# Kernel tuning notes

Measured on AMD Instinct MI355X. Metric: run time of the kernel, lower is better.

## Reference

```python
import jax, jax.numpy as jnp
import numpy as np

B, S, D, H = 2, 2048, 2048, 16
DK = D // H


def setup_inputs() -> dict:
    key = jax.random.key(0)
    k1, k2, k3 = jax.random.split(key, 3)
    x = jax.random.normal(k1, (B, S, D), dtype=jnp.float32)
    # trunc-normal in the original; plain normal with matching std is fine for a numeric baseline
    std_qkv = 2.0 / (DK + D)  # note: original passes variance as std to trunc_normal_
    W_qkv = jax.random.normal(k2, (3 * D, D), dtype=jnp.float32) * std_qkv
    W_o = jax.random.normal(k3, (D, D), dtype=jnp.float32) * (1.0 / D)
    return {"x": x, "W_qkv": W_qkv, "W_o": W_o}


def reference(x, W_qkv, W_o):
    b, s, d = x.shape
    # fused QKV projection: y = x @ W_qkv^T
    qkv = jnp.einsum('bsd,ed->bse', x, W_qkv)  # [b, s, 3d]
    q, k, v = jnp.split(qkv, 3, axis=-1)
    # [b, s, d] -> [b, h, s, dk]
    def to_heads(t):
        return t.reshape(b, s, H, DK).transpose(0, 2, 1, 3)
    q, k, v = to_heads(q), to_heads(k), to_heads(v)
    scores = jnp.einsum('bhqd,bhkd->bhqk', q, k) / np.sqrt(DK).astype(np.float32)
    causal = jnp.tril(jnp.ones((s, s), dtype=bool))
    scores = jnp.where(causal, scores, -jnp.inf)
    att = jax.nn.softmax(scores, axis=-1)
    out = jnp.einsum('bhqk,bhkd->bhqd', att, v)  # [b, h, s, dk]
    out = out.transpose(0, 2, 1, 3).reshape(b, s, d)
    return jnp.einsum('bsd,od->bso', out, W_o)
```

## Files before the change

kernel.cpp:

```cpp
#include <hip/hip_runtime.h>

typedef _Float16 f16;
typedef _Float16 f16x4 __attribute__((ext_vector_type(4)));
typedef _Float16 f16x8 __attribute__((ext_vector_type(8)));
typedef float    f32x4 __attribute__((ext_vector_type(4)));

#define MFMA_F16(a,b,c) __builtin_amdgcn_mfma_f32_16x16x32_f16((a),(b),(c),0,0,0)

static constexpr int B_  = 2;
static constexpr int S_  = 2048;
static constexpr int D_  = 2048;
static constexpr int H_  = 16;
static constexpr int DK_ = 128;
static constexpr int K_  = 2048;

__device__ __forceinline__ void gload_lds16(const void* g, void* l) {
  __builtin_amdgcn_global_load_lds(
      (const __attribute__((address_space(1))) void*)g,
      (__attribute__((address_space(3))) void*)l, 16, 0, 0);
}

__global__ __launch_bounds__(256) void cast_f16_kernel(const float* __restrict__ in,
                                                       f16* __restrict__ out, int n4) {
  int i = blockIdx.x * 256 + threadIdx.x;
  int stride = gridDim.x * 256;
  for (int j = i; j < n4; j += stride) {
    float4 v = reinterpret_cast<const float4*>(in)[j];
    f16x4 o = {(f16)v.x, (f16)v.y, (f16)v.z, (f16)v.w};
    reinterpret_cast<f16x4*>(out)[j] = o;
  }
}


__device__ __forceinline__ void stage_ph(const f16* gA, const f16* gB, int t,
                                         char* slot, int w) {
  gload_lds16(gA + (size_t)(w * 16) * K_ + t * 32,       slot + w * 1024);
  gload_lds16(gB + (size_t)(w * 16) * K_ + t * 32,       slot + 8192 + w * 1024);
  gload_lds16(gB + (size_t)((w + 8) * 16) * K_ + t * 32, slot + 8192 + (w + 8) * 1024);
}

__device__ __forceinline__ void mfma_ph(const char* slot, int aoff, int boff, int lro,
                                        f32x4 (&acc)[4][4]) {
  f16x8 af[4], bf[4];
#pragma unroll
  for (int mi = 0; mi < 4; ++mi)
    af[mi] = *(const f16x8*)(slot + aoff + mi * 1024 + lro);
#pragma unroll
  for (int ni = 0; ni < 4; ++ni)
    bf[ni] = *(const f16x8*)(slot + boff + ni * 1024 + lro);
  __builtin_amdgcn_s_setprio(1);
#pragma unroll
  for (int mi = 0; mi < 4; ++mi)
#pragma unroll
    for (int ni = 0; ni < 4; ++ni)
      acc[mi][ni] = MFMA_F16(af[mi], bf[ni], acc[mi][ni]);
  __builtin_amdgcn_s_setprio(0);
}

#define SYNCW(N)                                              \
  asm volatile("s_waitcnt vmcnt(" #N ")" ::: "memory");       \
  __builtin_amdgcn_s_barrier();                               \
  asm volatile("" ::: "memory");

__device__ __forceinline__ void gemm_core_w8(const f16* __restrict__ A,
                                             const f16* __restrict__ Bw,
                                             int brow, int bcol, char* lds,
                                             f32x4 (&acc)[4][4]) {
  const int tid = threadIdx.x;
  const int w = tid >> 6, l = tid & 63;
  const int lg = l >> 4, lr = l & 15;
  const int wm = w >> 2, wn = w & 3;
  const int lro = (lr * 4 + (lg ^ ((lr >> 1) & 3))) * 16;
  const int aoff = wm * 4096;
  const int boff = 8192 + wn * 4096;

#pragma unroll
  for (int mi = 0; mi < 4; ++mi)
#pragma unroll
    for (int ni = 0; ni < 4; ++ni) acc[mi][ni] = (f32x4){0.f, 0.f, 0.f, 0.f};

  const int kgsrc = (l & 3) ^ ((l >> 3) & 3);
  const f16* gA = A  + (size_t)(brow * 128 + (l >> 2)) * K_ + kgsrc * 8;
  const f16* gB = Bw + (size_t)(bcol * 256 + (l >> 2)) * K_ + kgsrc * 8;

  char* s0 = lds;
  char* s1 = lds + 24576;
  char* s2 = lds + 49152;
  char* s3 = lds + 73728;

  stage_ph(gA, gB, 0, s0, w);
  stage_ph(gA, gB, 1, s1, w);
  stage_ph(gA, gB, 2, s2, w);
  SYNCW(6)

  for (int tb = 0; tb < 15; ++tb) {
    const int t = tb * 4;
    stage_ph(gA, gB, t + 3, s3, w); mfma_ph(s0, aoff, boff, lro, acc); SYNCW(6)
    stage_ph(gA, gB, t + 4, s0, w); mfma_ph(s1, aoff, boff, lro, acc); SYNCW(6)
    stage_ph(gA, gB, t + 5, s1, w); mfma_ph(s2, aoff, boff, lro, acc); SYNCW(6)
    stage_ph(gA, gB, t + 6, s2, w); mfma_ph(s3, aoff, boff, lro, acc); SYNCW(6)
  }
  stage_ph(gA, gB, 63, s3, w); mfma_ph(s0, aoff, boff, lro, acc); SYNCW(6)
  mfma_ph(s1, aoff, boff, lro, acc); SYNCW(3)
  mfma_ph(s2, aoff, boff, lro, acc); SYNCW(0)
  mfma_ph(s3, aoff, boff, lro, acc);
}

__global__ __launch_bounds__(512) void gemm_qkv_kernel(const f16* __restrict__ xb,
                                                       const f16* __restrict__ wqkv,
                                                       f16* __restrict__ Q,
                                                       f16* __restrict__ Kk,
                                                       f16* __restrict__ Vt) {
  __shared__ __align__(16) char lds[98304];
  const int bid = blockIdx.x;
  const int xcd = bid & 7;
  const int local = bid >> 3;
  const int brow = xcd * 4 + (local & 3);
  const int bcol = local >> 2;

  f32x4 acc[4][4];
  gemm_core_w8(xb, wqkv, brow, bcol, lds, acc);

  const int tid = threadIdx.x;
  const int w = tid >> 6, l = tid & 63;
  const int lg = l >> 4, lr = l & 15;
  const int wm = w >> 2, wn = w & 3;

  const int which = bcol >> 3;
  const int nsec = (bcol & 7) * 256;

  if (which == 2) {
#pragma unroll
    for (int mi = 0; mi < 4; ++mi) {
      const int m0 = brow * 128 + wm * 64 + mi * 16 + lg * 4;
      const int b = m0 >> 11, s = m0 & 2047;
#pragma unroll
      for (int ni = 0; ni < 4; ++ni) {
        const int n = nsec + wn * 64 + ni * 16 + lr;
        const int h = n >> 7, dk = n & 127;
        f16x4 v = {(f16)acc[mi][ni][0], (f16)acc[mi][ni][1],
                   (f16)acc[mi][ni][2], (f16)acc[mi][ni][3]};
        *(f16x4*)(Vt + ((size_t)(b * H_ + h) * DK_ + dk) * S_ + s) = v;
      }
    }
  } else {
    f16* outp = (which == 0) ? Q : Kk;
    const float scale = (which == 0) ? 0.08838834764831845f : 1.0f;
#pragma unroll
    for (int mi = 0; mi < 4; ++mi) {
      const int m0 = brow * 128 + wm * 64 + mi * 16 + lg * 4;
#pragma unroll
      for (int ni = 0; ni < 4; ++ni) {
        const int n = nsec + wn * 64 + ni * 16 + lr;
        const int h = n >> 7, dk = n & 127;
#pragma unroll
        for (int r = 0; r < 4; ++r) {
          const int mm = m0 + r;
          const int b = mm >> 11, s = mm & 2047;
          outp[(((size_t)b * H_ + h) * S_ + s) * DK_ + dk] = (f16)(acc[mi][ni][r] * scale);
        }
      }
    }
  }
}

__global__ __launch_bounds__(512) void gemm_out_kernel(const f16* __restrict__ ab,
                                                       const f16* __restrict__ wo,
                                                       float* __restrict__ out) {
  __shared__ __align__(16) char lds[98304];
  const int bid = blockIdx.x;
  const int xcd = bid & 7;
  const int local = bid >> 3;
  const int brow = xcd * 4 + (local & 3);
  const int bcol = local >> 2;

  f32x4 acc[4][4];
  gemm_core_w8(ab, wo, brow, bcol, lds, acc);

  const int tid = threadIdx.x;
  const int w = tid >> 6, l = tid & 63;
  const int lg = l >> 4, lr = l & 15;
  const int wm = w >> 2, wn = w & 3;

#pragma unroll
  for (int mi = 0; mi < 4; ++mi) {
    const int m0 = brow * 128 + wm * 64 + mi * 16 + lg * 4;
#pragma unroll
    for (int ni = 0; ni < 4; ++ni) {
      const int n = bcol * 256 + wn * 64 + ni * 16 + lr;
#pragma unroll
      for (int r = 0; r < 4; ++r)
        out[(size_t)(m0 + r) * D_ + n] = acc[mi][ni][r];
    }
  }
}

__global__ __launch_bounds__(256) void attn_kernel(const f16* __restrict__ Q,
                                                   const f16* __restrict__ Kg,
                                                   const f16* __restrict__ Vt,
                                                   f16* __restrict__ O) {
  __shared__ __align__(16) unsigned char Ks[64 * 256];
  __shared__ __align__(16) unsigned char Vs[128 * 128];
  __shared__ __align__(16) unsigned char Ps[4][16 * 128];

  const int bid = blockIdx.x;
  const int pr = bid & 15;
  const int h  = (bid >> 4) & 15;
  const int b  = bid >> 8;
  const int bh = b * H_ + h;
  const int tid = threadIdx.x;
  const int w = tid >> 6, l = tid & 63;
  const int lg = l >> 4, lr = l & 15;

  for (int half = 0; half < 2; ++half) {
    const int qt = half ? (31 - pr) : pr;

    const f16* Qg = Q + ((size_t)bh * S_ + qt * 64 + w * 16) * DK_;
    f16x8 qf[4];
#pragma unroll
    for (int kd = 0; kd < 4; ++kd)
      qf[kd] = *(const f16x8*)(Qg + (size_t)lr * DK_ + kd * 32 + lg * 8);

    f32x4 o[8];
#pragma unroll
    for (int n = 0; n < 8; ++n) o[n] = (f32x4){0.f, 0.f, 0.f, 0.f};
    float mrun[4] = {-1e30f, -1e30f, -1e30f, -1e30f};
    float lrun[4] = {0.f, 0.f, 0.f, 0.f};

    const int ntiles = qt + 1;
    for (int kt = 0; kt < ntiles; ++kt) {
      __syncthreads();
      const f16* Kt = Kg + ((size_t)bh * S_ + kt * 64) * DK_;
#pragma unroll
      for (int i = 0; i < 4; ++i) {
        const int chunk = i * 256 + tid;
        const int row = chunk >> 4, c8 = chunk & 15;
        uint4 v = *(const uint4*)(Kt + (size_t)row * DK_ + c8 * 8);
        *(uint4*)(Ks + row * 256 + ((c8 * 16) ^ ((row & 7) << 4))) = v;
      }
      const f16* Vtt = Vt + (size_t)bh * DK_ * S_ + kt * 64;
#pragma unroll
      for (int i = 0; i < 4; ++i) {
        const int chunk = i * 256 + tid;
        const int row = chunk >> 3, c8 = chunk & 7;
        uint4 v = *(const uint4*)(Vtt + (size_t)row * S_ + c8 * 8);
        *(uint4*)(Vs + row * 128 + ((c8 * 16) ^ ((row & 7) << 4))) = v;
      }
      __syncthreads();

      f32x4 s[4];
#pragma unroll
      for (int j = 0; j < 4; ++j) s[j] = (f32x4){0.f, 0.f, 0.f, 0.f};
      __builtin_amdgcn_s_setprio(1);
#pragma unroll
      for (int j = 0; j < 4; ++j) {
        const int row = j * 16 + lr;
#pragma unroll
        for (int kd = 0; kd < 4; ++kd) {
          f16x8 kf = *(const f16x8*)(Ks + row * 256 + ((kd * 64 + lg * 16) ^ ((row & 7) << 4)));
          s[j] = MFMA_F16(qf[kd], kf, s[j]);
        }
      }
      __builtin_amdgcn_s_setprio(0);
      if (kt == qt) {
#pragma unroll
        for (int j = 0; j < 4; ++j) {
          const int col = j * 16 + lr;
#pragma unroll
          for (int r = 0; r < 4; ++r) {
            const int qrow = w * 16 + lg * 4 + r;
            if (col > qrow) s[j][r] = -1e30f;
          }
        }
      }
      float scl[4];
#pragma unroll
      for (int r = 0; r < 4; ++r) {
        float m0 = fmaxf(fmaxf(s[0][r], s[1][r]), fmaxf(s[2][r], s[3][r]));
#pragma unroll
        for (int msk = 1; msk < 16; msk <<= 1) m0 = fmaxf(m0, __shfl_xor(m0, msk, 64));
        const float nm = fmaxf(mrun[r], m0);
        scl[r] = __expf(mrun[r] - nm);
        mrun[r] = nm;
      }
      float rs[4] = {0.f, 0.f, 0.f, 0.f};
#pragma unroll
      for (int j = 0; j < 4; ++j) {
#pragma unroll
        for (int r = 0; r < 4; ++r) {
          const float p = __expf(fmaxf(s[j][r] - mrun[r], -80.f));
          rs[r] += p;
          const int row = lg * 4 + r;
          const int cb = (j * 16 + lr) * 2;
          *(f16*)(Ps[w] + row * 128 + (cb ^ ((row & 7) << 4))) = (f16)p;
        }
      }
#pragma unroll
      for (int r = 0; r < 4; ++r) {
        float t = rs[r];
#pragma unroll
        for (int msk = 1; msk < 16; msk <<= 1) t += __shfl_xor(t, msk, 64);
        lrun[r] = lrun[r] * scl[r] + t;
      }
#pragma unroll
      for (int n = 0; n < 8; ++n)
#pragma unroll
        for (int r = 0; r < 4; ++r) o[n][r] *= scl[r];

      asm volatile("s_waitcnt lgkmcnt(0)" ::: "memory");

      __builtin_amdgcn_s_setprio(1);
#pragma unroll
      for (int ks = 0; ks < 2; ++ks) {
        f16x8 pf = *(const f16x8*)(Ps[w] + lr * 128 + ((ks * 64 + lg * 16) ^ ((lr & 7) << 4)));
#pragma unroll
        for (int n = 0; n < 8; ++n) {
          const int row = n * 16 + lr;
          f16x8 vf = *(const f16x8*)(Vs + row * 128 + ((ks * 64 + lg * 16) ^ ((row & 7) << 4)));
          o[n] = MFMA_F16(pf, vf, o[n]);
        }
      }
      __builtin_amdgcn_s_setprio(0);
    }

#pragma unroll
    for (int r = 0; r < 4; ++r) {
      const float inv = 1.0f / lrun[r];
      const int srow = qt * 64 + w * 16 + lg * 4 + r;
      f16* op = O + ((size_t)b * S_ + srow) * D_ + h * DK_;
#pragma unroll
      for (int n = 0; n < 8; ++n) op[n * 16 + lr] = (f16)(o[n][r] * inv);
    }
  }
}

extern "C" void kernel_launch(void* const* d_in, const int* in_sizes, int n_in,
                              void* d_out, int out_size, void* d_ws, size_t ws_size,
                              hipStream_t stream) {
  const float* x    = (const float*)d_in[0];
  const float* wqkv = (const float*)d_in[1];
  const float* wo   = (const float*)d_in[2];
  float* out = (float*)d_out;
  char* ws = (char*)d_ws;

  f16* xb     = (f16*)(ws + 0);
  f16* wqkvb  = (f16*)(ws + 16777216);
  f16* wob    = (f16*)(ws + 41943040);
  f16* Qb     = (f16*)(ws + 50331648);
  f16* Kb     = (f16*)(ws + 67108864);
  f16* Vtb    = (f16*)(ws + 83886080);
  f16* attn_o = (f16*)(ws + 0);

  cast_f16_kernel<<<2048, 256, 0, stream>>>(x, xb, 8388608 / 4);
  cast_f16_kernel<<<2048, 256, 0, stream>>>(wqkv, wqkvb, 12582912 / 4);
  cast_f16_kernel<<<1024, 256, 0, stream>>>(wo, wob, 4194304 / 4);

  gemm_qkv_kernel<<<768, 512, 0, stream>>>(xb, wqkvb, Qb, Kb, Vtb);
  attn_kernel<<<512, 256, 0, stream>>>(Qb, Kb, Vtb, attn_o);
  gemm_out_kernel<<<256, 512, 0, stream>>>(attn_o, wob, out);
}
```

Before: 269.9 us.

## Shrink GEMM tiles to 128x128 with double buffering, prefetch attention K/V, merge casts

Both GEMMs move from 128x256 tiles with a 4-stage LDS pipeline to 128x128 tiles with a 64-wide K step and a two-slot double buffer. This halves LDS per block and doubles the grid, so more blocks can be resident per CU. The attention kernel now loads the next K/V tile into registers while computing on the current one, and the three cast launches become a single kernel. The trade-off is lower arithmetic intensity per tile, a full vmcnt(0) wait at every stage, and more register pressure in attention.

```diff
diff --git a/kernel.cpp b/kernel.cpp
--- a/kernel.cpp
+++ b/kernel.cpp
@@ -20,114 +20,127 @@
       (__attribute__((address_space(3))) void*)l, 16, 0, 0);
 }
 
-__global__ __launch_bounds__(256) void cast_f16_kernel(const float* __restrict__ in,
-                                                       f16* __restrict__ out, int n4) {
+__global__ __launch_bounds__(256) void cast_all_kernel(const float* __restrict__ x,
+                                                       const float* __restrict__ wqkv,
+                                                       const float* __restrict__ wo,
+                                                       f16* __restrict__ xb,
+                                                       f16* __restrict__ wqkvb,
+                                                       f16* __restrict__ wob) {
+  const int total = 6291456;
   int i = blockIdx.x * 256 + threadIdx.x;
   int stride = gridDim.x * 256;
-  for (int j = i; j < n4; j += stride) {
-    float4 v = reinterpret_cast<const float4*>(in)[j];
+  for (int j = i; j < total; j += stride) {
+    const float* src; f16* dst; int jj;
+    if (j < 2097152)      { src = x;    dst = xb;    jj = j; }
+    else if (j < 5242880) { src = wqkv; dst = wqkvb; jj = j - 2097152; }
+    else                  { src = wo;   dst = wob;   jj = j - 5242880; }
+    float4 v = reinterpret_cast<const float4*>(src)[jj];
     f16x4 o = {(f16)v.x, (f16)v.y, (f16)v.z, (f16)v.w};
-    reinterpret_cast<f16x4*>(out)[j] = o;
-  }
-}
-
-
-__device__ __forceinline__ void stage_ph(const f16* gA, const f16* gB, int t,
-                                         char* slot, int w) {
-  gload_lds16(gA + (size_t)(w * 16) * K_ + t * 32,       slot + w * 1024);
-  gload_lds16(gB + (size_t)(w * 16) * K_ + t * 32,       slot + 8192 + w * 1024);
-  gload_lds16(gB + (size_t)((w + 8) * 16) * K_ + t * 32, slot + 8192 + (w + 8) * 1024);
-}
-
-__device__ __forceinline__ void mfma_ph(const char* slot, int aoff, int boff, int lro,
-                                        f32x4 (&acc)[4][4]) {
-  f16x8 af[4], bf[4];
+    reinterpret_cast<f16x4*>(dst)[jj] = o;
+  }
+}
+
+
+#define SYNCW0                                          \
+  asm volatile("s_waitcnt vmcnt(0)" ::: "memory");      \
+  __builtin_amdgcn_s_barrier();                         \
+  asm volatile("" ::: "memory");
+
+__device__ __forceinline__ void stage2(const f16* gA, const f16* gB, char* slot, int w) {
+  gload_lds16(gA,      slot +         w * 1024);
+  gload_lds16(gA + 32, slot +  8192 + w * 1024);
+  gload_lds16(gB,      slot + 16384 + w * 1024);
+  gload_lds16(gB + 32, slot + 24576 + w * 1024);
+}
+
+__device__ __forceinline__ void compute2(const char* slot, int aoff, int boff, int lro,
+                                         f32x4 (&acc)[4][2]) {
+  f16x8 a0[4], b0[2], a1[4], b1[2];
+#pragma unroll
+  for (int mi = 0; mi < 4; ++mi) {
+    a0[mi] = *(const f16x8*)(slot +        aoff + mi * 1024 + lro);
+    a1[mi] = *(const f16x8*)(slot + 8192 + aoff + mi * 1024 + lro);
+  }
+#pragma unroll
+  for (int ni = 0; ni < 2; ++ni) {
+    b0[ni] = *(const f16x8*)(slot + 16384 + boff + ni * 1024 + lro);
+    b1[ni] = *(const f16x8*)(slot + 24576 + boff + ni * 1024 + lro);
+  }
+  __builtin_amdgcn_s_setprio(1);
 #pragma unroll
   for (int mi = 0; mi < 4; ++mi)
-    af[mi] = *(const f16x8*)(slot + aoff + mi * 1024 + lro);
-#pragma unroll
-  for (int ni = 0; ni < 4; ++ni)
-    bf[ni] = *(const f16x8*)(slot + boff + ni * 1024 + lro);
-  __builtin_amdgcn_s_setprio(1);
+#pragma unroll
+    for (int ni = 0; ni < 2; ++ni)
+      acc[mi][ni] = MFMA_F16(a0[mi], b0[ni], acc[mi][ni]);
 #pragma unroll
   for (int mi = 0; mi < 4; ++mi)
 #pragma unroll
-    for (int ni = 0; ni < 4; ++ni)
-      acc[mi][ni] = MFMA_F16(af[mi], bf[ni], acc[mi][ni]);
+    for (int ni = 0; ni < 2; ++ni)
+      acc[mi][ni] = MFMA_F16(a1[mi], b1[ni], acc[mi][ni]);
   __builtin_amdgcn_s_setprio(0);
 }
 
-#define SYNCW(N)                                              \
-  asm volatile("s_waitcnt vmcnt(" #N ")" ::: "memory");       \
-  __builtin_amdgcn_s_barrier();                               \
-  asm volatile("" ::: "memory");
-
-__device__ __forceinline__ void gemm_core_w8(const f16* __restrict__ A,
+__device__ __forceinline__ void gemm_core_db(const f16* __restrict__ A,
                                              const f16* __restrict__ Bw,
                                              int brow, int bcol, char* lds,
-                                             f32x4 (&acc)[4][4]) {
+                                             f32x4 (&acc)[4][2]) {
   const int tid = threadIdx.x;
   const int w = tid >> 6, l = tid & 63;
   const int lg = l >> 4, lr = l & 15;
   const int wm = w >> 2, wn = w & 3;
   const int lro = (lr * 4 + (lg ^ ((lr >> 1) & 3))) * 16;
   const int aoff = wm * 4096;
-  const int boff = 8192 + wn * 4096;
+  const int boff = wn * 2048;
 
 #pragma unroll
   for (int mi = 0; mi < 4; ++mi)
 #pragma unroll
-    for (int ni = 0; ni < 4; ++ni) acc[mi][ni] = (f32x4){0.f, 0.f, 0.f, 0.f};
+    for (int ni = 0; ni < 2; ++ni) acc[mi][ni] = (f32x4){0.f, 0.f, 0.f, 0.f};
 
   const int kgsrc = (l & 3) ^ ((l >> 3) & 3);
-  const f16* gA = A  + (size_t)(brow * 128 + (l >> 2)) * K_ + kgsrc * 8;
-  const f16* gB = Bw + (size_t)(bcol * 256 + (l >> 2)) * K_ + kgsrc * 8;
+  const f16* gA = A  + (size_t)(brow * 128 + w * 16 + (l >> 2)) * K_ + kgsrc * 8;
+  const f16* gB = Bw + (size_t)(bcol * 128 + w * 16 + (l >> 2)) * K_ + kgsrc * 8;
 
   char* s0 = lds;
-  char* s1 = lds + 24576;
-  char* s2 = lds + 49152;
-  char* s3 = lds + 73728;
-
-  stage_ph(gA, gB, 0, s0, w);
-  stage_ph(gA, gB, 1, s1, w);
-  stage_ph(gA, gB, 2, s2, w);
-  SYNCW(6)
-
-  for (int tb = 0; tb < 15; ++tb) {
-    const int t = tb * 4;
-    stage_ph(gA, gB, t + 3, s3, w); mfma_ph(s0, aoff, boff, lro, acc); SYNCW(6)
-    stage_ph(gA, gB, t + 4, s0, w); mfma_ph(s1, aoff, boff, lro, acc); SYNCW(6)
-    stage_ph(gA, gB, t + 5, s1, w); mfma_ph(s2, aoff, boff, lro, acc); SYNCW(6)
-    stage_ph(gA, gB, t + 6, s2, w); mfma_ph(s3, aoff, boff, lro, acc); SYNCW(6)
-  }
-  stage_ph(gA, gB, 63, s3, w); mfma_ph(s0, aoff, boff, lro, acc); SYNCW(6)
-  mfma_ph(s1, aoff, boff, lro, acc); SYNCW(3)
-  mfma_ph(s2, aoff, boff, lro, acc); SYNCW(0)
-  mfma_ph(s3, aoff, boff, lro, acc);
-}
-
-__global__ __launch_bounds__(512) void gemm_qkv_kernel(const f16* __restrict__ xb,
-                                                       const f16* __restrict__ wqkv,
-                                                       f16* __restrict__ Q,
-                                                       f16* __restrict__ Kk,
-                                                       f16* __restrict__ Vt) {
-  __shared__ __align__(16) char lds[98304];
+  char* s1 = lds + 32768;
+
+  stage2(gA, gB, s0, w);
+  SYNCW0
+
+  for (int tb = 0; tb < 16; ++tb) {
+    const int t = tb * 2;
+    stage2(gA + (size_t)(t + 1) * 64, gB + (size_t)(t + 1) * 64, s1, w);
+    compute2(s0, aoff, boff, lro, acc);
+    SYNCW0
+    if (tb < 15)
+      stage2(gA + (size_t)(t + 2) * 64, gB + (size_t)(t + 2) * 64, s0, w);
+    compute2(s1, aoff, boff, lro, acc);
+    SYNCW0
+  }
+}
+
+__global__ __launch_bounds__(512, 4) void gemm_qkv_kernel(const f16* __restrict__ xb,
+                                                          const f16* __restrict__ wqkv,
+                                                          f16* __restrict__ Q,
+                                                          f16* __restrict__ Kk,
+                                                          f16* __restrict__ Vt) {
+  __shared__ __align__(16) char lds[65536];
   const int bid = blockIdx.x;
   const int xcd = bid & 7;
   const int local = bid >> 3;
   const int brow = xcd * 4 + (local & 3);
   const int bcol = local >> 2;
 
-  f32x4 acc[4][4];
-  gemm_core_w8(xb, wqkv, brow, bcol, lds, acc);
+  f32x4 acc[4][2];
+  gemm_core_db(xb, wqkv, brow, bcol, lds, acc);
 
   const int tid = threadIdx.x;
   const int w = tid >> 6, l = tid & 63;
   const int lg = l >> 4, lr = l & 15;
   const int wm = w >> 2, wn = w & 3;
 
-  const int which = bcol >> 3;
-  const int nsec = (bcol & 7) * 256;
+  const int which = bcol >> 4;
+  const int h = bcol & 15;
 
   if (which == 2) {
 #pragma unroll
@@ -135,9 +148,8 @@
       const int m0 = brow * 128 + wm * 64 + mi * 16 + lg * 4;
       const int b = m0 >> 11, s = m0 & 2047;
 #pragma unroll
-      for (int ni = 0; ni < 4; ++ni) {
-        const int n = nsec + wn * 64 + ni * 16 + lr;
-        const int h = n >> 7, dk = n & 127;
+      for (int ni = 0; ni < 2; ++ni) {
+        const int dk = wn * 32 + ni * 16 + lr;
         f16x4 v = {(f16)acc[mi][ni][0], (f16)acc[mi][ni][1],
                    (f16)acc[mi][ni][2], (f16)acc[mi][ni][3]};
         *(f16x4*)(Vt + ((size_t)(b * H_ + h) * DK_ + dk) * S_ + s) = v;
@@ -150,9 +162,8 @@
     for (int mi = 0; mi < 4; ++mi) {
       const int m0 = brow * 128 + wm * 64 + mi * 16 + lg * 4;
 #pragma unroll
-      for (int ni = 0; ni < 4; ++ni) {
-        const int n = nsec + wn * 64 + ni * 16 + lr;
-        const int h = n >> 7, dk = n & 127;
+      for (int ni = 0; ni < 2; ++ni) {
+        const int dk = wn * 32 + ni * 16 + lr;
 #pragma unroll
         for (int r = 0; r < 4; ++r) {
           const int mm = m0 + r;
@@ -164,18 +175,18 @@
   }
 }
 
-__global__ __launch_bounds__(512) void gemm_out_kernel(const f16* __restrict__ ab,
-                                                       const f16* __restrict__ wo,
-                                                       float* __restrict__ out) {
-  __shared__ __align__(16) char lds[98304];
+__global__ __launch_bounds__(512, 4) void gemm_out_kernel(const f16* __restrict__ ab,
+                                                          const f16* __restrict__ wo,
+                                                          float* __restrict__ out) {
+  __shared__ __align__(16) char lds[65536];
   const int bid = blockIdx.x;
   const int xcd = bid & 7;
   const int local = bid >> 3;
   const int brow = xcd * 4 + (local & 3);
   const int bcol = local >> 2;
 
-  f32x4 acc[4][4];
-  gemm_core_w8(ab, wo, brow, bcol, lds, acc);
+  f32x4 acc[4][2];
+  gemm_core_db(ab, wo, brow, bcol, lds, acc);
 
   const int tid = threadIdx.x;
   const int w = tid >> 6, l = tid & 63;
@@ -186,8 +197,8 @@
   for (int mi = 0; mi < 4; ++mi) {
     const int m0 = brow * 128 + wm * 64 + mi * 16 + lg * 4;
 #pragma unroll
-    for (int ni = 0; ni < 4; ++ni) {
-      const int n = bcol * 256 + wn * 64 + ni * 16 + lr;
+    for (int ni = 0; ni < 2; ++ni) {
+      const int n = bcol * 128 + wn * 32 + ni * 16 + lr;
 #pragma unroll
       for (int r = 0; r < 4; ++r)
         out[(size_t)(m0 + r) * D_ + n] = acc[mi][ni][r];
@@ -195,10 +206,10 @@
   }
 }
 
-__global__ __launch_bounds__(256) void attn_kernel(const f16* __restrict__ Q,
-                                                   const f16* __restrict__ Kg,
-                                                   const f16* __restrict__ Vt,
-                                                   f16* __restrict__ O) {
+__global__ __launch_bounds__(256, 4) void attn_kernel(const f16* __restrict__ Q,
+                                                      const f16* __restrict__ Kg,
+                                                      const f16* __restrict__ Vt,
+                                                      f16* __restrict__ O) {
   __shared__ __align__(16) unsigned char Ks[64 * 256];
   __shared__ __align__(16) unsigned char Vs[128 * 128];
   __shared__ __align__(16) unsigned char Ps[4][16 * 128];
@@ -212,6 +223,9 @@
   const int w = tid >> 6, l = tid & 63;
   const int lg = l >> 4, lr = l & 15;
 
+  const f16* Kbase = Kg + (size_t)bh * S_ * DK_;
+  const f16* Vbase = Vt + (size_t)bh * DK_ * S_;
+
   for (int half = 0; half < 2; ++half) {
     const int qt = half ? (31 - pr) : pr;
 
@@ -228,25 +242,38 @@
     float lrun[4] = {0.f, 0.f, 0.f, 0.f};
 
     const int ntiles = qt + 1;
+
+    uint4 kreg[4], vreg[4];
+#pragma unroll
+    for (int i = 0; i < 4; ++i) {
+      const int chunk = i * 256 + tid;
+      const int krow = chunk >> 4, kc8 = chunk & 15;
+      kreg[i] = *(const uint4*)(Kbase + (size_t)krow * DK_ + kc8 * 8);
+      const int vrow = chunk >> 3, vc8 = chunk & 7;
+      vreg[i] = *(const uint4*)(Vbase + (size_t)vrow * S_ + vc8 * 8);
+    }
+
     for (int kt = 0; kt < ntiles; ++kt) {
       __syncthreads();
-      const f16* Kt = Kg + ((size_t)bh * S_ + kt * 64) * DK_;
 #pragma unroll
       for (int i = 0; i < 4; ++i) {
         const int chunk = i * 256 + tid;
-        const int row = chunk >> 4, c8 = chunk & 15;
-        uint4 v = *(const uint4*)(Kt + (size_t)row * DK_ + c8 * 8);
-        *(uint4*)(Ks + row * 256 + ((c8 * 16) ^ ((row & 7) << 4))) = v;
-      }
-      const f16* Vtt = Vt + (size_t)bh * DK_ * S_ + kt * 64;
-#pragma unroll
-      for (int i = 0; i < 4; ++i) {
-        const int chunk = i * 256 + tid;
-        const int row = chunk >> 3, c8 = chunk & 7;
-        uint4 v = *(const uint4*)(Vtt + (size_t)row * S_ + c8 * 8);
-        *(uint4*)(Vs + row * 128 + ((c8 * 16) ^ ((row & 7) << 4))) = v;
+        const int krow = chunk >> 4, kc8 = chunk & 15;
+        *(uint4*)(Ks + krow * 256 + ((kc8 * 16) ^ ((krow & 7) << 4))) = kreg[i];
+        const int vrow = chunk >> 3, vc8 = chunk & 7;
+        *(uint4*)(Vs + vrow * 128 + ((vc8 * 16) ^ ((vrow & 7) << 4))) = vreg[i];
       }
       __syncthreads();
+      if (kt + 1 < ntiles) {
+#pragma unroll
+        for (int i = 0; i < 4; ++i) {
+          const int chunk = i * 256 + tid;
+          const int krow = chunk >> 4, kc8 = chunk & 15;
+          kreg[i] = *(const uint4*)(Kbase + (size_t)((kt + 1) * 64 + krow) * DK_ + kc8 * 8);
+          const int vrow = chunk >> 3, vc8 = chunk & 7;
+          vreg[i] = *(const uint4*)(Vbase + (size_t)vrow * S_ + (kt + 1) * 64 + vc8 * 8);
+        }
+      }
 
       f32x4 s[4];
 #pragma unroll
@@ -351,11 +378,9 @@
   f16* Vtb    = (f16*)(ws + 83886080);
   f16* attn_o = (f16*)(ws + 0);
 
-  cast_f16_kernel<<<2048, 256, 0, stream>>>(x, xb, 8388608 / 4);
-  cast_f16_kernel<<<2048, 256, 0, stream>>>(wqkv, wqkvb, 12582912 / 4);
-  cast_f16_kernel<<<1024, 256, 0, stream>>>(wo, wob, 4194304 / 4);
-
-  gemm_qkv_kernel<<<768, 512, 0, stream>>>(xb, wqkvb, Qb, Kb, Vtb);
+  cast_all_kernel<<<2048, 256, 0, stream>>>(x, wqkv, wo, xb, wqkvb, wob);
+
+  gemm_qkv_kernel<<<1536, 512, 0, stream>>>(xb, wqkvb, Qb, Kb, Vtb);
   attn_kernel<<<512, 256, 0, stream>>>(Qb, Kb, Vtb, attn_o);
-  gemm_out_kernel<<<256, 512, 0, stream>>>(attn_o, wob, out);
-}
+  gemm_out_kernel<<<512, 512, 0, stream>>>(attn_o, wob, out);
+}
```

Measured after the change: 459.9 us. 1.7x slower.
